# Optimization experiments

Measured on AMD Instinct MI355X. Metric: run time of the kernel, lower is better.

The kernel has to match this reference:

```python
import jax, jax.numpy as jnp
import numpy as np
import math

F, H, N_CURR = 16384, 64, 8192
BOUNDARY = -0.01


def setup_inputs() -> dict:
    key = jax.random.key(0)
    ks = jax.random.split(key, 12)
    he_w = math.sqrt(2.0 / (H + 1))
    he_t = math.sqrt(2.0)
    return {
        "X": jax.random.normal(ks[0], (F,), jnp.float32),
        "delta": jax.random.uniform(ks[1], (F,), jnp.float32),
        "Ht": jax.random.normal(ks[2], (F, H), jnp.float32),
        "c_t": jax.random.normal(ks[3], (H,), jnp.float32),
        "c_global": jax.random.normal(ks[4], (F, H), jnp.float32),
        "lstm_weights": he_w * jax.random.normal(ks[5], (F, 3 * H, H + 1), jnp.float32),
        "lstm_bias": jnp.zeros((F, 3 * H), jnp.float32),
        "lstm_xT_weights": he_t * jax.random.normal(ks[6], (F, 2 * H, 1), jnp.float32),
        "lstm_xT_bias": jnp.zeros((F, 2 * H), jnp.float32),
        "lstm_delT_weights": he_t * jax.random.normal(ks[7], (F, 3 * H, 1), jnp.float32),
        "lstm_c_inp_weights": jax.random.normal(ks[8], (F, H), jnp.float32),
        "lstm_c_out_weights": jax.random.normal(ks[9], (F, H), jnp.float32),
        "feat_idx": jnp.arange(N_CURR, dtype=jnp.int32),
    }


def reference(X, delta, Ht, c_t, c_global, lstm_weights, lstm_bias,
              lstm_xT_weights, lstm_xT_bias, lstm_delT_weights,
              lstm_c_inp_weights, lstm_c_out_weights, feat_idx):
    # weight constraint on the hidden_size-th row of delT weights (clip to <= boundary)
    delT_w = lstm_delT_weights.at[:, H, :].set(
        jnp.minimum(lstm_delT_weights[:, H, :], BOUNDARY))

    x = X[feat_idx]                                   # [n]
    h_prev = Ht[feat_idx]                             # [n, H]
    cur_input = jnp.concatenate([x[:, None], h_prev], axis=-1)   # [n, H+1]

    # gathered per-feature small matvecs
    cur_out = jnp.einsum('ngh,nh->ng', lstm_weights[feat_idx], cur_input) \
        + lstm_bias[feat_idx]                          # [n, 3H]
    xm_out = lstm_xT_weights[feat_idx, :, 0] * x[:, None] + lstm_xT_bias[feat_idx]   # [n, 2H]
    dT_out = delT_w[feat_idx, :, 0] * delta[feat_idx][:, None]                        # [n, 3H]

    gate_input, gate_output, gate_pre_c = jnp.split(cur_out, 3, axis=-1)
    xm_T1, xm_T2 = jnp.split(xm_out, 2, axis=-1)
    del_T1, del_T2, del_To = jnp.split(dT_out, 3, axis=-1)

    T_1t = jax.nn.sigmoid(xm_T1 + jax.nn.sigmoid(del_T1))
    T_2t = jax.nn.sigmoid(xm_T2 + jax.nn.sigmoid(del_T2))
    gate_input = jax.nn.sigmoid(gate_input + lstm_c_inp_weights[feat_idx] * c_t)
    gate_pre_c = jnp.tanh(gate_pre_c)

    c_tilde = (1.0 - gate_input * T_1t) * c_t + gate_input * T_1t * gate_pre_c
    c_new = (1.0 - gate_input) * c_t + gate_input * T_2t * gate_pre_c
    gate_output = jax.nn.sigmoid(
        gate_output + lstm_c_out_weights[feat_idx] * c_tilde + del_To)

    h_new = gate_output * jnp.tanh(c_tilde)            # [n, H]

    H_curr = jnp.zeros_like(Ht).at[feat_idx].set(h_new)     # scatter into [F, H]
    c_global_new = c_global.at[feat_idx].set(c_new)
    C_curr = jnp.mean(c_new, axis=0)                   # aggregate_by='Mean' -> [H]
    return H_curr, c_global_new, C_curr
```

## Files before the change

kernel.cpp:

```cpp
#include <hip/hip_runtime.h>
#include <cstdint>
#include <cstddef>

#define HH 64
#define G2 128
#define G3 192
#define ROWF 12480
#define CHF 2080
#define BOUNDARY (-0.01f)

__device__ __forceinline__ float sigm(float x) { return 1.0f / (1.0f + __expf(-x)); }

__device__ __forceinline__ void load_lds16_nt(const float* g, float* l) {
    __builtin_amdgcn_global_load_lds(
        (const __attribute__((address_space(1))) void*)g,
        (__attribute__((address_space(3))) void*)l, 16, 0, 2);
}

__global__ __launch_bounds__(256) void init_tail(float* __restrict__ outH,
                                                 float* __restrict__ outC,
                                                 const float* __restrict__ c_global,
                                                 int base4, int cnt4) {
    int idx = blockIdx.x * 256 + threadIdx.x;
    int stride = gridDim.x * 256;
    for (int k = idx; k < cnt4; k += stride) {
        ((float4*)outH)[base4 + k] = make_float4(0.f, 0.f, 0.f, 0.f);
        ((float4*)outC)[base4 + k] = ((const float4*)c_global)[base4 + k];
    }
}

__global__ __launch_bounds__(256) void lstm_main(
    const float* __restrict__ X, const float* __restrict__ delta,
    const float* __restrict__ Ht, const float* __restrict__ c_t,
    const float* __restrict__ W, const float* __restrict__ bias,
    const float* __restrict__ xTw, const float* __restrict__ xTb,
    const float* __restrict__ dTw, const float* __restrict__ cinw,
    const float* __restrict__ coutw, const int* __restrict__ feat_idx,
    float* __restrict__ outH, float* __restrict__ outC,
    unsigned int* __restrict__ counter, int use_ws) {

    __shared__ float w[3 * CHF];
    __shared__ float inp[72];
    __shared__ float co[96];

    const int t    = threadIdx.x;
    const int b    = blockIdx.x;
    const int f    = b >> 1;
    const int hb   = (b & 1) << 5;
    const int i    = feat_idx[f];
    const int lane = t & 63;
    const int wv   = t >> 6;

    if (use_ws && b == 0 && t == 0) *counter = 0u;

    const size_t i1 = (size_t)i * HH;
    const size_t i2 = (size_t)i * G2;
    const size_t i3 = (size_t)i * G3;

    float xi = 0.f, di = 0.f, ct = 0.f, cinv = 0.f, coutv = 0.f;
    float xw1 = 0.f, xw2 = 0.f, xb1 = 0.f, xb2 = 0.f;
    float dw1 = 0.f, dw2 = 0.f, dwo = 0.f, bv = 0.f;
    if (t < 32) {
        const int h = hb + t;
        xi   = X[i];
        di   = delta[i];
        ct   = c_t[h];
        cinv = cinw[i1 + h];
        coutv = coutw[i1 + h];
        xw1  = xTw[i2 + h];
        xw2  = xTw[i2 + HH + h];
        xb1  = xTb[i2 + h];
        xb2  = xTb[i2 + HH + h];
        dw1  = dTw[i3 + h];
        dw2  = dTw[i3 + HH + h];
        dwo  = dTw[i3 + 2 * HH + h];
    }
    if (t < 96) {
        const int ch = t >> 5, idx = t & 31;
        bv = bias[i3 + ch * HH + hb + idx];
    }

    if (t == 0) inp[0] = X[i];
    if (wv == 1) inp[1 + lane] = Ht[i1 + lane];

    const float* wrow = W + (size_t)i * ROWF;
    for (int s = wv; s < 27; s += 4) {
        const int ch  = s / 9;
        const int off = s % 9;
        const int fl  = off * 256 + lane * 4;
        if (fl < CHF)
            load_lds16_nt(wrow + (size_t)(64 * ch + hb) * 65 + fl,
                          &w[ch * CHF + off * 256]);
    }
    __syncthreads();

    if (t < 96) {
        const int ch = t >> 5, idx = t & 31;
        const float* wr = &w[ch * CHF + idx * 65];
        float acc = bv;
        #pragma unroll
        for (int k = 0; k < 65; ++k) acc = fmaf(wr[k], inp[k], acc);
        co[t] = acc;
    }
    __syncthreads();

    if (t < 32) {
        const int h = hb + t;
        float gi_pre = co[t];
        float go_pre = co[32 + t];
        float gc     = tanhf(co[64 + t]);

        float xm1 = fmaf(xw1, xi, xb1);
        float xm2 = fmaf(xw2, xi, xb2);
        if (h == 0) dw2 = fminf(dw2, BOUNDARY);

        float T1 = sigm(xm1 + sigm(dw1 * di));
        float T2 = sigm(xm2 + sigm(dw2 * di));
        float gi = sigm(gi_pre + cinv * ct);

        float gT1     = gi * T1;
        float c_tilde = (1.f - gT1) * ct + gT1 * gc;
        float c_new   = (1.f - gi) * ct + gi * T2 * gc;
        float go      = sigm(go_pre + coutv * c_tilde + dwo * di);

        outH[i1 + h] = go * tanhf(c_tilde);
        outC[i1 + h] = c_new;
    }
}

__global__ __launch_bounds__(256) void creduce(
    const float* __restrict__ outC, const int* __restrict__ feat_idx,
    float* __restrict__ s2, unsigned int* __restrict__ counter,
    float* __restrict__ outM, int n, int rp)
{
    __shared__ float s[256];
    __shared__ int islast;
    const int b = blockIdx.x, t = threadIdx.x;
    const int h = t & 63, g = t >> 6;
    const int r1 = min(n, (b + 1) * rp);
    float acc = 0.f;
    for (int r = b * rp + g; r < r1; r += 4)
        acc += outC[(size_t)feat_idx[r] * HH + h];
    s[t] = acc;
    __syncthreads();
    if (t < HH) s2[(size_t)b * HH + h] = s[h] + s[64+h] + s[128+h] + s[192+h];
    __threadfence();
    __syncthreads();
    if (t == 0) {
        unsigned old = atomicAdd(counter, 1u);
        islast = (old == gridDim.x - 1) ? 1 : 0;
    }
    __syncthreads();
    if (islast) {
        __threadfence();
        if (t < HH) {
            float tot = 0.f;
            for (int b2 = 0; b2 < (int)gridDim.x; ++b2) tot += s2[(size_t)b2 * HH + h];
            outM[h] = tot / (float)n;
        }
        if (t == 0) *counter = 0u;
    }
}

__global__ __launch_bounds__(256) void reduceAll(const float* __restrict__ outC,
                                                 const int* __restrict__ feat_idx,
                                                 float* __restrict__ outM, int n) {
    __shared__ float s[256];
    const int t = threadIdx.x, h = t & 63, g = t >> 6;
    float acc = 0.f;
    for (int r = g; r < n; r += 4)
        acc += outC[(size_t)feat_idx[r] * HH + h];
    s[t] = acc;
    __syncthreads();
    if (t < HH) outM[h] = (s[h] + s[64+h] + s[128+h] + s[192+h]) / (float)n;
}

extern "C" void kernel_launch(void* const* d_in, const int* in_sizes, int n_in,
                              void* d_out, int out_size, void* d_ws, size_t ws_size,
                              hipStream_t stream) {
    const float* X        = (const float*)d_in[0];
    const float* delta    = (const float*)d_in[1];
    const float* Ht       = (const float*)d_in[2];
    const float* c_t      = (const float*)d_in[3];
    const float* c_global = (const float*)d_in[4];
    const float* W        = (const float*)d_in[5];
    const float* bias     = (const float*)d_in[6];
    const float* xTw      = (const float*)d_in[7];
    const float* xTb      = (const float*)d_in[8];
    const float* dTw      = (const float*)d_in[9];
    const float* cinw     = (const float*)d_in[10];
    const float* coutw    = (const float*)d_in[11];
    const int*   feat_idx = (const int*)d_in[12];

    const int F  = in_sizes[0];
    const int n  = in_sizes[12];
    const int FH = F * HH;

    float* out  = (float*)d_out;
    float* outH = out;
    float* outC = out + FH;
    float* outM = out + 2 * FH;

    const size_t need = (64 * HH + 64) * sizeof(float);
    const int use_ws = (ws_size >= need) ? 1 : 0;
    float* s2 = (float*)d_ws;
    unsigned int* counter = (unsigned int*)(s2 + 64 * HH);

    if (F > n) {
        int base4 = n * (HH / 4);
        int cnt4  = (F - n) * (HH / 4);
        int blocks = (cnt4 + 255) / 256;
        if (blocks > 512) blocks = 512;
        init_tail<<<blocks, 256, 0, stream>>>(outH, outC, c_global, base4, cnt4);
    }

    lstm_main<<<2 * n, 256, 0, stream>>>(X, delta, Ht, c_t, W, bias, xTw, xTb,
                                         dTw, cinw, coutw, feat_idx, outH, outC,
                                         counter, use_ws);

    if (use_ws) {
        int rp = (n + 63) / 64;
        creduce<<<64, 256, 0, stream>>>(outC, feat_idx, s2, counter, outM, n, rp);
    } else {
        reduceAll<<<1, 256, 0, stream>>>(outC, feat_idx, outM, n);
    }
}
```

Baseline: 108.7 us.

## Replace LDS-staged matvec with direct float4 register loads and shuffle reductions

The main LSTM kernel now uses one block per feature instead of two. It drops the global-to-LDS staging of weight rows and the per-thread 65-element serial dot product. Each 16-lane group instead reads float4-aligned weight segments directly from global memory, handles the unaligned row-start and row-end elements specially, and reduces partial sums with cross-lane shuffles. The goal is to avoid the LDS round trip and spread the matvec across all 256 threads, at the cost of extra shuffles and alignment-dependent branches.

Result: slower. 149.6 us (+37.7%).

```diff
diff --git a/kernel.cpp b/kernel.cpp
--- a/kernel.cpp
+++ b/kernel.cpp
@@ -5,17 +5,12 @@
 #define HH 64
 #define G2 128
 #define G3 192
+#define WROW 65
 #define ROWF 12480
-#define CHF 2080
 #define BOUNDARY (-0.01f)
+#define NRED 64
 
 __device__ __forceinline__ float sigm(float x) { return 1.0f / (1.0f + __expf(-x)); }
-
-__device__ __forceinline__ void load_lds16_nt(const float* g, float* l) {
-    __builtin_amdgcn_global_load_lds(
-        (const __attribute__((address_space(1))) void*)g,
-        (__attribute__((address_space(3))) void*)l, 16, 0, 2);
-}
 
 __global__ __launch_bounds__(256) void init_tail(float* __restrict__ outH,
                                                  float* __restrict__ outC,
@@ -29,7 +24,7 @@
     }
 }
 
-__global__ __launch_bounds__(256) void lstm_main(
+__global__ __launch_bounds__(256) void lstm_vec(
     const float* __restrict__ X, const float* __restrict__ delta,
     const float* __restrict__ Ht, const float* __restrict__ c_t,
     const float* __restrict__ W, const float* __restrict__ bias,
@@ -37,94 +32,97 @@
     const float* __restrict__ dTw, const float* __restrict__ cinw,
     const float* __restrict__ coutw, const int* __restrict__ feat_idx,
     float* __restrict__ outH, float* __restrict__ outC,
-    unsigned int* __restrict__ counter, int use_ws) {
-
-    __shared__ float w[3 * CHF];
-    __shared__ float inp[72];
-    __shared__ float co[96];
-
-    const int t    = threadIdx.x;
-    const int b    = blockIdx.x;
-    const int f    = b >> 1;
-    const int hb   = (b & 1) << 5;
-    const int i    = feat_idx[f];
-    const int lane = t & 63;
-    const int wv   = t >> 6;
+    unsigned int* __restrict__ counter, int use_ws)
+{
+    __shared__ float inp[68];
+    __shared__ float co[G3];
+
+    const int t  = threadIdx.x;
+    const int b  = blockIdx.x;
+    const int i  = feat_idx[b];
+    const int g  = t >> 4;
+    const int j  = t & 15;
+    const int phi = g & 3;
+    const int c0  = (4 - phi) & 3;
 
     if (use_ws && b == 0 && t == 0) *counter = 0u;
 
     const size_t i1 = (size_t)i * HH;
-    const size_t i2 = (size_t)i * G2;
-    const size_t i3 = (size_t)i * G3;
-
-    float xi = 0.f, di = 0.f, ct = 0.f, cinv = 0.f, coutv = 0.f;
-    float xw1 = 0.f, xw2 = 0.f, xb1 = 0.f, xb2 = 0.f;
-    float dw1 = 0.f, dw2 = 0.f, dwo = 0.f, bv = 0.f;
-    if (t < 32) {
-        const int h = hb + t;
-        xi   = X[i];
-        di   = delta[i];
-        ct   = c_t[h];
-        cinv = cinw[i1 + h];
-        coutv = coutw[i1 + h];
-        xw1  = xTw[i2 + h];
-        xw2  = xTw[i2 + HH + h];
-        xb1  = xTb[i2 + h];
-        xb2  = xTb[i2 + HH + h];
-        dw1  = dTw[i3 + h];
-        dw2  = dTw[i3 + HH + h];
-        dwo  = dTw[i3 + 2 * HH + h];
-    }
-    if (t < 96) {
-        const int ch = t >> 5, idx = t & 31;
-        bv = bias[i3 + ch * HH + hb + idx];
-    }
-
+
+    if (t < HH) inp[1 + t] = Ht[i1 + t];
     if (t == 0) inp[0] = X[i];
-    if (wv == 1) inp[1 + lane] = Ht[i1 + lane];
-
-    const float* wrow = W + (size_t)i * ROWF;
-    for (int s = wv; s < 27; s += 4) {
-        const int ch  = s / 9;
-        const int off = s % 9;
-        const int fl  = off * 256 + lane * 4;
-        if (fl < CHF)
-            load_lds16_nt(wrow + (size_t)(64 * ch + hb) * 65 + fl,
-                          &w[ch * CHF + off * 256]);
-    }
-    __syncthreads();
-
-    if (t < 96) {
-        const int ch = t >> 5, idx = t & 31;
-        const float* wr = &w[ch * CHF + idx * 65];
-        float acc = bv;
-        #pragma unroll
-        for (int k = 0; k < 65; ++k) acc = fmaf(wr[k], inp[k], acc);
-        co[t] = acc;
-    }
-    __syncthreads();
-
-    if (t < 32) {
-        const int h = hb + t;
-        float gi_pre = co[t];
-        float go_pre = co[32 + t];
-        float gc     = tanhf(co[64 + t]);
-
-        float xm1 = fmaf(xw1, xi, xb1);
-        float xm2 = fmaf(xw2, xi, xb2);
-        if (h == 0) dw2 = fminf(dw2, BOUNDARY);
+    __syncthreads();
+
+    float iv0, iv1, iv2, iv3;
+    {
+        const int c = c0 + 4 * j;
+        iv0 = (c     <= 64) ? inp[c]     : 0.f;
+        iv1 = (c + 1 <= 64) ? inp[c + 1] : 0.f;
+        iv2 = (c + 2 <= 64) ? inp[c + 2] : 0.f;
+        iv3 = (c + 3 <= 64) ? inp[c + 3] : 0.f;
+    }
+    float hin0 = inp[0], hin1 = inp[1], hin2 = inp[2], in64 = inp[64];
+
+    const float* wbase = W + (size_t)i * ROWF;
+
+    #pragma unroll 2
+    for (int k = 0; k < 12; ++k) {
+        const int r = g + 16 * k;
+        const size_t base = (size_t)r * WROW;
+        const float4 wv = *(const float4*)(wbase + base + c0 + 4 * j);
+        float acc = wv.x * iv0;
+        acc = fmaf(wv.y, iv1, acc);
+        acc = fmaf(wv.z, iv2, acc);
+        acc = fmaf(wv.w, iv3, acc);
+        if (j == 0) {
+            if (phi == 0) {
+                acc = fmaf(wbase[base + 64], in64, acc);
+            } else {
+                const float4 hv = *(const float4*)(wbase + base - phi);
+                const float hf[4] = {hv.x, hv.y, hv.z, hv.w};
+                if (0 < c0) acc = fmaf(hf[phi + 0], hin0, acc);
+                if (1 < c0) acc = fmaf(hf[phi + 1], hin1, acc);
+                if (2 < c0) acc = fmaf(hf[phi + 2], hin2, acc);
+            }
+        }
+        acc += __shfl_xor(acc, 1, 16);
+        acc += __shfl_xor(acc, 2, 16);
+        acc += __shfl_xor(acc, 4, 16);
+        acc += __shfl_xor(acc, 8, 16);
+        if (j == 0) co[r] = acc;
+    }
+    __syncthreads();
+
+    if (t < HH) {
+        const size_t i2 = (size_t)i * G2;
+        const size_t i3 = (size_t)i * G3;
+        const float xi = inp[0];
+        const float di = delta[i];
+        const float ct = c_t[t];
+
+        float gi_pre = co[t]          + bias[i3 + t];
+        float go_pre = co[HH + t]     + bias[i3 + HH + t];
+        float gc     = tanhf(co[2*HH + t] + bias[i3 + 2*HH + t]);
+
+        float xm1 = fmaf(xTw[i2 + t],      xi, xTb[i2 + t]);
+        float xm2 = fmaf(xTw[i2 + HH + t], xi, xTb[i2 + HH + t]);
+
+        float dw1 = dTw[i3 + t];
+        float dw2 = dTw[i3 + HH + t];
+        if (t == 0) dw2 = fminf(dw2, BOUNDARY);
+        float dwo = dTw[i3 + 2 * HH + t];
 
         float T1 = sigm(xm1 + sigm(dw1 * di));
         float T2 = sigm(xm2 + sigm(dw2 * di));
-        float gi = sigm(gi_pre + cinv * ct);
+        float gi = sigm(gi_pre + cinw[i1 + t] * ct);
 
         float gT1     = gi * T1;
         float c_tilde = (1.f - gT1) * ct + gT1 * gc;
         float c_new   = (1.f - gi) * ct + gi * T2 * gc;
-        float go      = sigm(go_pre + coutv * c_tilde + dwo * di);
-
-        outH[i1 + h] = go * tanhf(c_tilde);
-        outC[i1 + h] = c_new;
+        float go      = sigm(go_pre + coutw[i1 + t] * c_tilde + dwo * di);
+
+        outH[i1 + t] = go * tanhf(c_tilde);
+        outC[i1 + t] = c_new;
     }
 }
 
@@ -201,10 +199,10 @@
     float* outC = out + FH;
     float* outM = out + 2 * FH;
 
-    const size_t need = (64 * HH + 64) * sizeof(float);
+    const size_t need = (NRED * HH + 64) * sizeof(float);
     const int use_ws = (ws_size >= need) ? 1 : 0;
     float* s2 = (float*)d_ws;
-    unsigned int* counter = (unsigned int*)(s2 + 64 * HH);
+    unsigned int* counter = (unsigned int*)(s2 + NRED * HH);
 
     if (F > n) {
         int base4 = n * (HH / 4);
@@ -214,13 +212,13 @@
         init_tail<<<blocks, 256, 0, stream>>>(outH, outC, c_global, base4, cnt4);
     }
 
-    lstm_main<<<2 * n, 256, 0, stream>>>(X, delta, Ht, c_t, W, bias, xTw, xTb,
-                                         dTw, cinw, coutw, feat_idx, outH, outC,
-                                         counter, use_ws);
+    lstm_vec<<<n, 256, 0, stream>>>(X, delta, Ht, c_t, W, bias, xTw, xTb,
+                                    dTw, cinw, coutw, feat_idx, outH, outC,
+                                    counter, use_ws);
 
     if (use_ws) {
-        int rp = (n + 63) / 64;
-        creduce<<<64, 256, 0, stream>>>(outC, feat_idx, s2, counter, outM, n, rp);
+        int rp = (n + NRED - 1) / NRED;
+        creduce<<<NRED, 256, 0, stream>>>(outC, feat_idx, s2, counter, outM, n, rp);
     } else {
         reduceAll<<<1, 256, 0, stream>>>(outC, feat_idx, outM, n);
     }
```
